# Kernel optimization log

Hardware: AMD Instinct MI355X
Metric: run time of the kernel (lower is better)

## Reference

```python
import jax, jax.numpy as jnp
import numpy as np
import math

HIDDEN = 512
N_PROTO = 1024
BATCH = 16384


def setup_inputs() -> dict:
    key = jax.random.key(0)
    kx, kp = jax.random.split(key)
    X = jax.random.normal(kx, (BATCH, HIDDEN), dtype=jnp.float32)
    # prototypes init: uniform in [-k, k], k = 1/sqrt(hidden)
    k = 1.0 / math.sqrt(HIDDEN)
    u = jax.random.uniform(kp, (N_PROTO, HIDDEN), dtype=jnp.float32)
    prototypes = k + (-2.0 * k) * u
    return {"X": X, "prototypes": prototypes}


def reference(X, prototypes):
    # out[b, p] = -sum_h (X[b,h] - prototypes[p,h])^2
    x_sq = jnp.sum(X * X, axis=1, keepdims=True)            # [B, 1]
    p_sq = jnp.sum(prototypes * prototypes, axis=1)[None, :]  # [1, P]
    cross = jnp.einsum("bh,ph->bp", X, prototypes)          # [B, P]
    return -(x_sq + p_sq - 2.0 * cross)
```

## Files before the change

kernel.cpp:

```cpp
#include <hip/hip_runtime.h>
#include <hip/hip_bf16.h>

#define MDIM 16384
#define NDIM 1024
#define KDIM 512
#define BM 256
#define BN 256
#define BK 64
#define KTILES (KDIM / BK)

typedef __attribute__((ext_vector_type(8))) short bf16x8;
typedef __attribute__((ext_vector_type(4))) float f32x4;

__device__ __forceinline__ short f2bf(float f) {
    union { float f; unsigned u; } v; v.f = f;
    unsigned r = v.u + 0x7fff + ((v.u >> 16) & 1);
    return (short)(r >> 16);
}

__device__ __forceinline__ bf16x8 cvt8(float4 a, float4 b) {
    bf16x8 o;
    o[0] = f2bf(a.x); o[1] = f2bf(a.y); o[2] = f2bf(a.z); o[3] = f2bf(a.w);
    o[4] = f2bf(b.x); o[5] = f2bf(b.y); o[6] = f2bf(b.z); o[7] = f2bf(b.w);
    return o;
}

__device__ __forceinline__ void gload_lds16(const void* g, void* l) {
    __builtin_amdgcn_global_load_lds(
        (const __attribute__((address_space(1))) void*)g,
        (__attribute__((address_space(3))) void*)l, 16, 0, 0);
}

__global__ __launch_bounds__(256) void convert_sumsq(
        const float* __restrict__ X, const float* __restrict__ P,
        short* __restrict__ Xbf, short* __restrict__ Pbf,
        float* __restrict__ xsq, float* __restrict__ psq) {
    int wave = (blockIdx.x * blockDim.x + threadIdx.x) >> 6;
    int lane = threadIdx.x & 63;
    const float* src; short* dstb; float* dsts; int row;
    if (wave < MDIM) { src = X; dstb = Xbf; dsts = xsq; row = wave; }
    else             { src = P; dstb = Pbf; dsts = psq; row = wave - MDIM; }
    const float4* r4 = (const float4*)(src + (size_t)row * KDIM) + lane * 2;
    float4 a = r4[0], b = r4[1];
    *(bf16x8*)(dstb + (size_t)row * KDIM + lane * 8) = cvt8(a, b);
    float s = a.x*a.x + a.y*a.y + a.z*a.z + a.w*a.w
            + b.x*b.x + b.y*b.y + b.z*b.z + b.w*b.w;
    #pragma unroll
    for (int off = 32; off; off >>= 1) s += __shfl_down(s, off, 64);
    if (lane == 0) dsts[row] = s;
}

__global__ __launch_bounds__(512, 2) void dist_gemm_bf2(
        const short* __restrict__ Xbf, const short* __restrict__ Pbf,
        const float* __restrict__ xsq, const float* __restrict__ psq,
        float* __restrict__ out) {
    __shared__ short As[2][BM * BK];
    __shared__ short Bs[2][BN * BK];

    int tid = threadIdx.x;
    int bid = blockIdx.x;
    int swz = (bid & 7) * 32 + (bid >> 3);
    int bn = swz & 3, bm = swz >> 2;
    int row0 = bm * BM, col0 = bn * BN;

    int lane = tid & 63, wid = tid >> 6;
    int wr = wid >> 2, wc = wid & 3;

    f32x4 acc[8][4] = {};

    const short* Ab = Xbf + (size_t)row0 * KDIM;
    const short* Bb = Pbf + (size_t)col0 * KDIM;

    auto stage = [&](int sel, int kt) {
        #pragma unroll
        for (int i = 0; i < 4; ++i) {
            int c = tid + 512 * i;
            int row = c >> 3;
            int g16 = (c & 7) ^ (row & 7);
            const char* ga = (const char*)(Ab + (size_t)row * KDIM)
                             + kt * (BK * 2) + g16 * 16;
            const char* gb = (const char*)(Bb + (size_t)row * KDIM)
                             + kt * (BK * 2) + g16 * 16;
            char* la = (char*)&As[sel][0] + i * 8192 + wid * 1024;
            char* lb = (char*)&Bs[sel][0] + i * 8192 + wid * 1024;
            gload_lds16(ga, la);
            gload_lds16(gb, lb);
        }
    };

    auto compute = [&](int sel) {
        #pragma unroll
        for (int ks = 0; ks < 2; ++ks) {
            int kb = ks * 64 + ((lane >> 4) * 16);
            bf16x8 bfr[4];
            #pragma unroll
            for (int n = 0; n < 4; ++n) {
                int row = wc * 64 + n * 16 + (lane & 15);
                int off = (row * (BK * 2) + kb) ^ ((row & 7) << 4);
                bfr[n] = *(const bf16x8*)((const char*)&Bs[sel][0] + off);
            }
            #pragma unroll
            for (int m = 0; m < 8; ++m) {
                int row = wr * 128 + m * 16 + (lane & 15);
                int off = (row * (BK * 2) + kb) ^ ((row & 7) << 4);
                bf16x8 af = *(const bf16x8*)((const char*)&As[sel][0] + off);
                #pragma unroll
                for (int n = 0; n < 4; ++n)
                    acc[m][n] = __builtin_amdgcn_mfma_f32_16x16x32_bf16(
                        af, bfr[n], acc[m][n], 0, 0, 0);
            }
        }
    };

    stage(0, 0);
    __syncthreads();
    int cur = 0;
    for (int kt = 0; kt < KTILES - 1; ++kt) {
        stage(cur ^ 1, kt + 1);
        compute(cur);
        __syncthreads();
        cur ^= 1;
    }
    compute(cur);

    int cr = (lane >> 4) * 4;
    int cc = lane & 15;
    float ps[4];
    #pragma unroll
    for (int n = 0; n < 4; ++n) ps[n] = psq[col0 + wc * 64 + n * 16 + cc];
    #pragma unroll
    for (int m = 0; m < 8; ++m) {
        int grb = row0 + wr * 128 + m * 16 + cr;
        #pragma unroll
        for (int r = 0; r < 4; ++r) {
            float xv = xsq[grb + r];
            size_t ob = (size_t)(grb + r) * NDIM;
            #pragma unroll
            for (int n = 0; n < 4; ++n) {
                int gc = col0 + wc * 64 + n * 16 + cc;
                out[ob + gc] = 2.0f * acc[m][n][r] - xv - ps[n];
            }
        }
    }
}

__global__ __launch_bounds__(256) void sumsq_kernel(
        const float* __restrict__ X, const float* __restrict__ P,
        float* __restrict__ xsq, float* __restrict__ psq) {
    int wave = (blockIdx.x * blockDim.x + threadIdx.x) >> 6;
    int lane = threadIdx.x & 63;
    const float* src; float* dst; int row;
    if (wave < MDIM) { src = X; dst = xsq; row = wave; }
    else             { src = P; dst = psq; row = wave - MDIM; }
    const float4* r4 = (const float4*)(src + (size_t)row * KDIM) + lane * 2;
    float4 a = r4[0], b = r4[1];
    float s = a.x*a.x + a.y*a.y + a.z*a.z + a.w*a.w
            + b.x*b.x + b.y*b.y + b.z*b.z + b.w*b.w;
    #pragma unroll
    for (int off = 32; off; off >>= 1) s += __shfl_down(s, off, 64);
    if (lane == 0) dst[row] = s;
}

__global__ __launch_bounds__(256) void dist_gemm(
        const float* __restrict__ X, const float* __restrict__ P,
        const float* __restrict__ xsq, const float* __restrict__ psq,
        float* __restrict__ out) {
    __shared__ short As[128 * BK];
    __shared__ short Bs[128 * BK];
    int tid = threadIdx.x;
    int bid = blockIdx.x;
    int swz = (bid & 7) * 128 + (bid >> 3);
    int bn = swz & 7, bm = swz >> 3;
    int row0 = bm * 128, col0 = bn * 128;
    int lane = tid & 63, wid = tid >> 6;
    int wm = (wid >> 1) * 64, wn = (wid & 1) * 64;
    f32x4 acc[4][4] = {};
    int rbase = tid >> 3;
    int kg = tid & 7;
    const float* Abase = X + (size_t)row0 * KDIM;
    const float* Bbase = P + (size_t)col0 * KDIM;
    for (int kt = 0; kt < KDIM / BK; ++kt) {
        int kofs = kt * BK + kg * 8;
        __syncthreads();
        #pragma unroll
        for (int i = 0; i < 4; ++i) {
            int row = rbase + 32 * i;
            const float4* ga = (const float4*)(Abase + (size_t)row * KDIM + kofs);
            float4 a0 = ga[0], a1 = ga[1];
            const float4* gb = (const float4*)(Bbase + (size_t)row * KDIM + kofs);
            float4 b0 = gb[0], b1 = gb[1];
            int off = (row * (BK * 2) + kg * 16) ^ ((row & 7) << 4);
            *(bf16x8*)((char*)As + off) = cvt8(a0, a1);
            *(bf16x8*)((char*)Bs + off) = cvt8(b0, b1);
        }
        __syncthreads();
        #pragma unroll
        for (int ks = 0; ks < 2; ++ks) {
            bf16x8 af[4], bfr[4];
            int kb = ks * 64 + ((lane >> 4) * 16);
            #pragma unroll
            for (int m = 0; m < 4; ++m) {
                int row = wm + m * 16 + (lane & 15);
                int off = (row * (BK * 2) + kb) ^ ((row & 7) << 4);
                af[m] = *(const bf16x8*)((const char*)As + off);
            }
            #pragma unroll
            for (int n = 0; n < 4; ++n) {
                int row = wn + n * 16 + (lane & 15);
                int off = (row * (BK * 2) + kb) ^ ((row & 7) << 4);
                bfr[n] = *(const bf16x8*)((const char*)Bs + off);
            }
            #pragma unroll
            for (int m = 0; m < 4; ++m)
                #pragma unroll
                for (int n = 0; n < 4; ++n)
                    acc[m][n] = __builtin_amdgcn_mfma_f32_16x16x32_bf16(
                        af[m], bfr[n], acc[m][n], 0, 0, 0);
        }
    }
    int cr = (lane >> 4) * 4;
    int cc = lane & 15;
    #pragma unroll
    for (int n = 0; n < 4; ++n) {
        int gc = col0 + wn + n * 16 + cc;
        float ps = psq[gc];
        #pragma unroll
        for (int m = 0; m < 4; ++m) {
            int grb = row0 + wm + m * 16 + cr;
            #pragma unroll
            for (int r = 0; r < 4; ++r) {
                float v = 2.0f * acc[m][n][r] - xsq[grb + r] - ps;
                out[(size_t)(grb + r) * NDIM + gc] = v;
            }
        }
    }
}

extern "C" void kernel_launch(void* const* d_in, const int* in_sizes, int n_in,
                              void* d_out, int out_size, void* d_ws, size_t ws_size,
                              hipStream_t stream) {
    const float* X = (const float*)d_in[0];
    const float* P = (const float*)d_in[1];
    float* out = (float*)d_out;

    const size_t bf_elems = (size_t)(MDIM + NDIM) * KDIM;
    const size_t need = bf_elems * 2 + (size_t)(MDIM + NDIM) * 4;

    if (ws_size >= need) {
        short* Xbf = (short*)d_ws;
        short* Pbf = Xbf + (size_t)MDIM * KDIM;
        float* xsq = (float*)(Xbf + bf_elems);
        float* psq = xsq + MDIM;
        convert_sumsq<<<(MDIM + NDIM) / 4, 256, 0, stream>>>(X, P, Xbf, Pbf, xsq, psq);
        dist_gemm_bf2<<<(MDIM / BM) * (NDIM / BN), 512, 0, stream>>>(Xbf, Pbf, xsq, psq, out);
    } else {
        float* xsq = (float*)d_ws;
        float* psq = xsq + MDIM;
        sumsq_kernel<<<(MDIM + NDIM) / 4, 256, 0, stream>>>(X, P, xsq, psq);
        dist_gemm<<<(MDIM / 128) * (NDIM / 128), 256, 0, stream>>>(X, P, xsq, psq, out);
    }
}
```

Baseline: 40.02 us.

## Interleave split A/B prefetch with MFMA phases using barriers and setprio

Restructures the bf16 GEMM main loop into a ping-pong schedule. Each k-subtile's MFMA work is split into two half-M phases, and the next tile's A and B global-to-LDS loads are issued between them. Explicit s_barrier and s_setprio calls are meant to keep the waves in lockstep and favour MFMA issue while loads are in flight. This replaces a single load-compute-syncthreads loop. In exchange it adds more barriers per k-tile and relies on a hand-placed vmcnt wait, which adds synchronisation overhead and the risk of hazards.

```diff
diff --git a/kernel.cpp b/kernel.cpp
--- a/kernel.cpp
+++ b/kernel.cpp
@@ -50,7 +50,7 @@
     if (lane == 0) dsts[row] = s;
 }
 
-__global__ __launch_bounds__(512, 2) void dist_gemm_bf2(
+__global__ __launch_bounds__(512, 2) void dist_gemm8(
         const short* __restrict__ Xbf, const short* __restrict__ Pbf,
         const float* __restrict__ xsq, const float* __restrict__ psq,
         float* __restrict__ out) {
@@ -71,57 +71,101 @@
     const short* Ab = Xbf + (size_t)row0 * KDIM;
     const short* Bb = Pbf + (size_t)col0 * KDIM;
 
-    auto stage = [&](int sel, int kt) {
+    auto stageA = [&](int sel, int kt) {
         #pragma unroll
         for (int i = 0; i < 4; ++i) {
             int c = tid + 512 * i;
             int row = c >> 3;
             int g16 = (c & 7) ^ (row & 7);
             const char* ga = (const char*)(Ab + (size_t)row * KDIM)
-                             + kt * (BK * 2) + g16 * 16;
+                             + (size_t)kt * (BK * 2) + g16 * 16;
+            gload_lds16(ga, (char*)&As[sel][0] + i * 8192 + wid * 1024);
+        }
+    };
+    auto stageB = [&](int sel, int kt) {
+        #pragma unroll
+        for (int i = 0; i < 4; ++i) {
+            int c = tid + 512 * i;
+            int row = c >> 3;
+            int g16 = (c & 7) ^ (row & 7);
             const char* gb = (const char*)(Bb + (size_t)row * KDIM)
-                             + kt * (BK * 2) + g16 * 16;
-            char* la = (char*)&As[sel][0] + i * 8192 + wid * 1024;
-            char* lb = (char*)&Bs[sel][0] + i * 8192 + wid * 1024;
-            gload_lds16(ga, la);
-            gload_lds16(gb, lb);
+                             + (size_t)kt * (BK * 2) + g16 * 16;
+            gload_lds16(gb, (char*)&Bs[sel][0] + i * 8192 + wid * 1024);
         }
     };
 
-    auto compute = [&](int sel) {
+    auto lds_off = [&](int row, int kb) {
+        return (row * (BK * 2) + kb) ^ ((row & 7) << 4);
+    };
+
+    auto ktile = [&](int sel, int kt) {
+        const char* asB = (const char*)&As[sel][0];
+        const char* bsB = (const char*)&Bs[sel][0];
+        bool more = (kt + 1) < KTILES;
+        bf16x8 bfr[4];
         #pragma unroll
         for (int ks = 0; ks < 2; ++ks) {
             int kb = ks * 64 + ((lane >> 4) * 16);
-            bf16x8 bfr[4];
-            #pragma unroll
-            for (int n = 0; n < 4; ++n) {
-                int row = wc * 64 + n * 16 + (lane & 15);
-                int off = (row * (BK * 2) + kb) ^ ((row & 7) << 4);
-                bfr[n] = *(const bf16x8*)((const char*)&Bs[sel][0] + off);
-            }
-            #pragma unroll
-            for (int m = 0; m < 8; ++m) {
-                int row = wr * 128 + m * 16 + (lane & 15);
-                int off = (row * (BK * 2) + kb) ^ ((row & 7) << 4);
-                bf16x8 af = *(const bf16x8*)((const char*)&As[sel][0] + off);
+            {
+                bf16x8 af[4];
+                #pragma unroll
+                for (int j = 0; j < 4; ++j)
+                    af[j] = *(const bf16x8*)(asB +
+                        lds_off(wr * 128 + j * 16 + (lane & 15), kb));
                 #pragma unroll
                 for (int n = 0; n < 4; ++n)
-                    acc[m][n] = __builtin_amdgcn_mfma_f32_16x16x32_bf16(
-                        af, bfr[n], acc[m][n], 0, 0, 0);
+                    bfr[n] = *(const bf16x8*)(bsB +
+                        lds_off(wc * 64 + n * 16 + (lane & 15), kb));
+                if (ks == 0 && more) stageA(sel ^ 1, kt + 1);
+                __builtin_amdgcn_s_barrier();
+                __builtin_amdgcn_s_setprio(1);
+                #pragma unroll
+                for (int j = 0; j < 4; ++j)
+                    #pragma unroll
+                    for (int n = 0; n < 4; ++n)
+                        acc[j][n] = __builtin_amdgcn_mfma_f32_16x16x32_bf16(
+                            af[j], bfr[n], acc[j][n], 0, 0, 0);
+                __builtin_amdgcn_s_setprio(0);
+                __builtin_amdgcn_s_barrier();
+            }
+            {
+                bf16x8 af[4];
+                #pragma unroll
+                for (int j = 0; j < 4; ++j)
+                    af[j] = *(const bf16x8*)(asB +
+                        lds_off(wr * 128 + 64 + j * 16 + (lane & 15), kb));
+                if (ks == 0 && more) stageB(sel ^ 1, kt + 1);
+                __builtin_amdgcn_s_barrier();
+                __builtin_amdgcn_s_setprio(1);
+                #pragma unroll
+                for (int j = 0; j < 4; ++j)
+                    #pragma unroll
+                    for (int n = 0; n < 4; ++n)
+                        acc[4 + j][n] = __builtin_amdgcn_mfma_f32_16x16x32_bf16(
+                            af[j], bfr[n], acc[4 + j][n], 0, 0, 0);
+                __builtin_amdgcn_s_setprio(0);
+                if (ks == 1) {
+                    if (more) asm volatile("s_waitcnt vmcnt(0)" ::: "memory");
+                    __builtin_amdgcn_s_barrier();
+                    __builtin_amdgcn_sched_barrier(0);
+                } else {
+                    __builtin_amdgcn_s_barrier();
+                }
             }
         }
     };
 
-    stage(0, 0);
-    __syncthreads();
-    int cur = 0;
-    for (int kt = 0; kt < KTILES - 1; ++kt) {
-        stage(cur ^ 1, kt + 1);
-        compute(cur);
-        __syncthreads();
-        cur ^= 1;
-    }
-    compute(cur);
+    stageA(0, 0);
+    stageB(0, 0);
+    asm volatile("s_waitcnt vmcnt(0)" ::: "memory");
+    __builtin_amdgcn_s_barrier();
+    __builtin_amdgcn_sched_barrier(0);
+
+    #pragma unroll 1
+    for (int p = 0; p < KTILES / 2; ++p) {
+        ktile(0, 2 * p);
+        ktile(1, 2 * p + 1);
+    }
 
     int cr = (lane >> 4) * 4;
     int cc = lane & 15;
@@ -252,7 +296,7 @@
         float* xsq = (float*)(Xbf + bf_elems);
         float* psq = xsq + MDIM;
         convert_sumsq<<<(MDIM + NDIM) / 4, 256, 0, stream>>>(X, P, Xbf, Pbf, xsq, psq);
-        dist_gemm_bf2<<<(MDIM / BM) * (NDIM / BN), 512, 0, stream>>>(Xbf, Pbf, xsq, psq, out);
+        dist_gemm8<<<(MDIM / BM) * (NDIM / BN), 512, 0, stream>>>(Xbf, Pbf, xsq, psq, out);
     } else {
         float* xsq = (float*)d_ws;
         float* psq = xsq + MDIM;
```

New measurement: 42.14 us. 1.05x slower.
